# Kernel tuning notes

Hardware: AMD Instinct MI355X
Metric: run time of the kernel (lower is better)

## Reference

```python
import jax, jax.numpy as jnp
import numpy as np

EPS_GN = 1e-8
EPS_ATTN = 1e-8


def setup_inputs() -> dict:
    key = jax.random.key(0)
    ks = jax.random.split(key, 13)
    B, C, N = 4, 512, 2048
    s = 0.02
    return {
        "x": jax.random.normal(ks[0], (B, C, N), jnp.float32),
        "dw_w": jax.random.normal(ks[1], (C, 3), jnp.float32) * s,
        "pw_w": jax.random.normal(ks[2], (C, C), jnp.float32) * s,
        "u_w": jax.random.normal(ks[3], (2 * C, C), jnp.float32) * s,
        "u_b": jax.random.normal(ks[4], (2 * C,), jnp.float32) * s,
        "v_w": jax.random.normal(ks[5], (2 * C, C), jnp.float32) * s,
        "v_b": jax.random.normal(ks[6], (2 * C,), jnp.float32) * s,
        "h_w": jax.random.normal(ks[7], (C, C), jnp.float32) * s,
        "h_b": jax.random.normal(ks[8], (C,), jnp.float32) * s,
        "q_w": jax.random.normal(ks[9], (C, C), jnp.float32) * s,
        "k_w": jax.random.normal(ks[10], (C, C), jnp.float32) * s,
        "o_w": jax.random.normal(ks[11], (C, 2 * C), jnp.float32) * s,
        "o_b": jax.random.normal(ks[12], (C,), jnp.float32) * s,
    }


def reference(x, dw_w, pw_w, u_w, u_b, v_w, v_b, h_w, h_b, q_w, k_w, o_w, o_b):
    # x: [B, C, N]
    C = x.shape[1]
    # GroupNorm(1, C): normalize over (C, N) per sample; affine is identity-init
    # in torch but we follow the module math with default weight=1, bias=0
    mean = jnp.mean(x, axis=(1, 2), keepdims=True)
    var = jnp.var(x, axis=(1, 2), keepdims=True)
    z = (x - mean) * jax.lax.rsqrt(var + EPS_GN)

    # local depthwise conv k=3, pad=1 (cross-correlation), no bias
    zp = jnp.pad(z, ((0, 0), (0, 0), (1, 1)))
    dw = (dw_w[:, 0, None] * zp[:, :, :-2]
          + dw_w[:, 1, None] * zp[:, :, 1:-1]
          + dw_w[:, 2, None] * zp[:, :, 2:])
    # pointwise conv (no bias)
    z = z + jnp.einsum('oc,bcn->bon', pw_w, dw)

    u = jax.nn.sigmoid(jnp.einsum('oc,bcn->bon', u_w, z) + u_b[:, None])  # [B,2C,N]
    v = jnp.einsum('oc,bcn->bon', v_w, z) + v_b[:, None]                  # [B,2C,N]
    h = jnp.einsum('oc,bcn->bno', h_w, z) + h_b                           # [B,N,C]

    q = h @ q_w.T  # [B,N,C]
    k = h @ k_w.T  # [B,N,C]
    scale = 1.0 / jnp.sqrt(jnp.float32(C))

    logits = jnp.einsum('bnc,bmc->bnm', q, k) * scale
    a = jax.nn.relu(logits)
    a = a * a
    a = a / (jnp.sum(a, axis=-1, keepdims=True) + EPS_ATTN)

    av = jnp.einsum('bnm,bom->bon', a, v)  # [B,2C,N]
    y = jnp.einsum('oc,bcn->bon', o_w, u * av) + o_b[:, None]
    return x + y
```

## Files before the change

kernel.cpp:

```cpp
#include <hip/hip_runtime.h>
#include <hip/hip_bf16.h>
#include <cstdint>

typedef __bf16 bhalf;
typedef __bf16 bhalf8 __attribute__((ext_vector_type(8)));
typedef float f32x4 __attribute__((ext_vector_type(4)));

enum { EPI_Z2=0, EPI_UV=1, EPI_BIAS=2, EPI_QK=3, EPI_ATTN=4, EPI_PV=5, EPI_Y=6 };

__device__ __forceinline__ void gl_lds16(const bhalf* g, bhalf* l) {
  __builtin_amdgcn_global_load_lds(
      (const __attribute__((address_space(1))) unsigned int*)g,
      (__attribute__((address_space(3))) unsigned int*)l,
      16, 0, 0);
}
__device__ __forceinline__ void barrier_raw() { asm volatile("s_barrier" ::: "memory"); }
#define VMW(n)  asm volatile("s_waitcnt vmcnt(" #n ")" ::: "memory")
#define LGKM0() asm volatile("s_waitcnt lgkmcnt(0)" ::: "memory")


template<int EPI>
__global__ void __launch_bounds__(512, 2)
g8(const bhalf* __restrict__ A, const bhalf* __restrict__ Bw,
   void* __restrict__ Out, void* __restrict__ Out2,
   const float* __restrict__ bias, const float* __restrict__ bias2,
   int N, int K, long sA, long sB, long sO, long sAuxf, float scale)
{
  constexpr int ASL = 256*64;
  constexpr int ABUF = 2*ASL;
  constexpr int STRIDE = 2*ABUF;
  __shared__ __align__(16) char lds[2*STRIDE];

  const int gx = gridDim.x, gy = gridDim.y;
  const int nwg = gx*gy;
  const int flat = blockIdx.y*gx + blockIdx.x;
  const int q8 = nwg>>3, r8 = nwg&7, xcd = flat&7, o8 = flat>>3;
  const int wsw = (xcd<r8 ? xcd*(q8+1) : r8*(q8+1)+(xcd-r8)*q8) + o8;
  const int bx = wsw % gx, by = wsw / gx;
  const int m0 = by*256, n0 = bx*256;
  const int bz = blockIdx.z;

  const bhalf* Ab = A + (long)bz*sA;
  const bhalf* Bb = Bw + (long)bz*sB;

  const int tid = threadIdx.x, wid = tid>>6, lane = tid&63;
  const int lm = lane&15, kq = lane>>4;
  const int wm = wid>>2, wn = wid&3;
  const int srow = lane>>2;
  const int csw = ((lane&3) ^ ((lane>>3)&3)) * 8;
  const int kqs = kq ^ ((lm>>1)&3);

  f32x4 acc[8][4];
  #pragma unroll
  for (int i=0;i<8;i++)
    #pragma unroll
    for (int j=0;j<4;j++) acc[i][j] = f32x4{0.f,0.f,0.f,0.f};

  auto stage = [&](int buf, int t){
    char* base = lds + buf*STRIDE;
    const int k0 = t*64;
    #pragma unroll
    for (int ksl=0; ksl<2; ksl++){
      #pragma unroll
      for (int c=0;c<2;c++){
        bhalf* dA = (bhalf*)(base + ksl*ASL + (wid*32 + c*16)*64);
        gl_lds16(Ab + (long)(m0 + wid*32 + c*16 + srow)*K + k0 + ksl*32 + csw, dA);
        bhalf* dB = (bhalf*)(base + ABUF + ksl*ASL + (wid*32 + c*16)*64);
        gl_lds16(Bb + (long)(n0 + wid*32 + c*16 + srow)*K + k0 + ksl*32 + csw, dB);
      }
    }
  };

  auto compute = [&](int buf){
    char* base = lds + buf*STRIDE;
    #pragma unroll
    for (int ks=0; ks<2; ks++){
      bhalf8 af[8], bf[4];
      #pragma unroll
      for (int i=0;i<8;i++)
        af[i] = *(const bhalf8*)(base + ks*ASL + (wm*128 + i*16 + lm)*64 + kqs*16);
      #pragma unroll
      for (int j=0;j<4;j++)
        bf[j] = *(const bhalf8*)(base + ABUF + ks*ASL + (wn*64 + j*16 + lm)*64 + kqs*16);
      __builtin_amdgcn_s_setprio(1);
      #pragma unroll
      for (int i=0;i<8;i++)
        #pragma unroll
        for (int j=0;j<4;j++)
          acc[i][j] = __builtin_amdgcn_mfma_f32_16x16x32_bf16(af[i], bf[j], acc[i][j], 0,0,0);
      __builtin_amdgcn_s_setprio(0);
    }
  };

  const int NT = K>>6;
  stage(0,0);
  for (int t=0; t<NT; ++t){
    if (t+1<NT){ stage((t+1)&1, t+1); VMW(8); }
    else       { VMW(0); }
    barrier_raw();
    compute(t&1);
    barrier_raw();
  }

  char* obase; int ldb;
  const float* bv = nullptr; int bc0 = 0; bool sig = false;
  if constexpr (EPI==EPI_ATTN){
    obase = (char*)Out + 2*((long)bz*sO + (long)m0*N + n0); ldb = N*2;
  }
  if constexpr (EPI==EPI_UV){
    bool uh = n0 < 1024; sig = uh;
    obase = (char*)(uh?Out:Out2) + 2*((long)m0*1024 + (n0 - (uh?0:1024)));
    ldb = 2048; bv = uh ? bias : bias2; bc0 = uh ? n0 : n0-1024;
  }

  float rs[8][4];
  if constexpr (EPI==EPI_ATTN){
    #pragma unroll
    for (int i=0;i<8;i++)
      #pragma unroll
      for (int r=0;r<4;r++) rs[i][r]=0.f;
  }
  #pragma unroll
  for (int i=0;i<8;i++){
    #pragma unroll
    for (int j=0;j<4;j++){
      const int lcol = wn*64 + j*16 + lm;
      #pragma unroll
      for (int r=0;r<4;r++){
        const int lrow = wm*128 + i*16 + kq*4 + r;
        float v = acc[i][j][r];
        if constexpr (EPI==EPI_ATTN){
          v *= scale; v = fmaxf(v,0.f); v = v*v;
          rs[i][r] += v;
        }
        if constexpr (EPI==EPI_UV){
          v += bv[bc0 + lcol];
          if (sig) v = 1.f/(1.f + __expf(-v));
        }
        const int cb = lcol*2;
        const int lb = lrow*512 + (((cb>>5) ^ ((lrow>>2)&3))<<5) + (cb&31);
        *(bhalf*)(lds + lb) = (bhalf)v;
      }
    }
  }
  if constexpr (EPI==EPI_ATTN){
    float* rd = (float*)Out2;
    #pragma unroll
    for (int i=0;i<8;i++){
      const int rbase = m0 + wm*128 + i*16 + kq*4;
      #pragma unroll
      for (int r=0;r<4;r++){
        float s = rs[i][r];
        s += __shfl_xor(s,1); s += __shfl_xor(s,2);
        s += __shfl_xor(s,4); s += __shfl_xor(s,8);
        if (lm==0) atomicAdd(rd + (long)bz*sAuxf + rbase + r, s);
      }
    }
  }
  LGKM0();
  barrier_raw();
  #pragma unroll
  for (int it=0; it<16; ++it){
    const int g = (it*512 + tid)*16;
    const int row = g >> 9, off = g & 511;
    const int lb = row*512 + (((off>>5) ^ ((row>>2)&3))<<5) + (off&31);
    uint4 val = *(const uint4*)(lds + lb);
    *(uint4*)(obase + (long)row*ldb + off) = val;
  }
  (void)scale; (void)bias; (void)bias2; (void)N;
}

template<int EPI>
__global__ void __launch_bounds__(256, 2)
g4(const bhalf* __restrict__ A, const bhalf* __restrict__ Bw,
   void* __restrict__ Out, void* __restrict__ Out2,
   const bhalf* __restrict__ auxb, const float* __restrict__ auxf,
   int N, int K, long sA, long sB, long sO, float scale, int rowshift)
{
  constexpr int ABUF = 256*64;
  constexpr int BBUF = 128*64;
  constexpr int STRIDE = ABUF + BBUF;
  __shared__ __align__(16) char lds[3*STRIDE];

  const int gx = gridDim.x, gy = gridDim.y;
  const int nwg = gx*gy;
  const int flat = blockIdx.y*gx + blockIdx.x;
  const int q8 = nwg>>3, r8 = nwg&7, xcd = flat&7, o8 = flat>>3;
  const int wsw = (xcd<r8 ? xcd*(q8+1) : r8*(q8+1)+(xcd-r8)*q8) + o8;
  const int bx = wsw % gx, by = wsw / gx;
  const int m0 = by*256, n0 = bx*128;
  const int bz = blockIdx.z;

  const bhalf* Ab = A + (long)bz*sA;
  const bhalf* Bb = Bw + (rowshift ? (long)(m0>>rowshift)*sB : (long)bz*sB);

  const int tid = threadIdx.x, wid = tid>>6, lane = tid&63;
  const int lm = lane&15, kq = lane>>4;
  const int wm = wid>>1, wn = wid&1;
  const int srow = lane>>2;
  const int csw = ((lane&3) ^ ((lane>>3)&3)) * 8;
  const int kqs = kq ^ ((lm>>1)&3);

  f32x4 acc[8][4];
  #pragma unroll
  for (int i=0;i<8;i++)
    #pragma unroll
    for (int j=0;j<4;j++) acc[i][j] = f32x4{0.f,0.f,0.f,0.f};

  auto stage = [&](int buf, int t){
    char* base = lds + buf*STRIDE;
    const int k0 = t*32;
    #pragma unroll
    for (int c=0;c<4;c++){
      bhalf* dA = (bhalf*)(base + (wid*64 + c*16)*64);
      gl_lds16(Ab + (long)(m0 + wid*64 + c*16 + srow)*K + k0 + csw, dA);
    }
    #pragma unroll
    for (int c=0;c<2;c++){
      bhalf* dB = (bhalf*)(base + ABUF + (wid*32 + c*16)*64);
      gl_lds16(Bb + (long)(n0 + wid*32 + c*16 + srow)*K + k0 + csw, dB);
    }
  };

  auto compute = [&](int buf){
    char* base = lds + buf*STRIDE;
    bhalf8 af[8], bf[4];
    #pragma unroll
    for (int i=0;i<8;i++)
      af[i] = *(const bhalf8*)(base + (wm*128 + i*16 + lm)*64 + kqs*16);
    #pragma unroll
    for (int j=0;j<4;j++)
      bf[j] = *(const bhalf8*)(base + ABUF + (wn*64 + j*16 + lm)*64 + kqs*16);
    __builtin_amdgcn_s_setprio(1);
    #pragma unroll
    for (int i=0;i<8;i++)
      #pragma unroll
      for (int j=0;j<4;j++)
        acc[i][j] = __builtin_amdgcn_mfma_f32_16x16x32_bf16(af[i], bf[j], acc[i][j], 0,0,0);
    __builtin_amdgcn_s_setprio(0);
  };

  const int NT = K>>5;
  stage(0,0); stage(1,1);
  int b0 = 0;
  for (int t=0; t<NT; ++t){
    if (t+2<NT){
      int b2 = b0+2; if (b2>=3) b2-=3;
      stage(b2, t+2);
      VMW(12);
    } else if (t+1<NT) { VMW(6); }
    else               { VMW(0); }
    barrier_raw();
    compute(b0);
    barrier_raw();
    if (++b0==3) b0=0;
  }

  char* obase; int ldb;
  if constexpr (EPI==EPI_PV){
    obase = (char*)Out + 2*((long)m0*1024 + n0); ldb = 2048;
  }
  if constexpr (EPI==EPI_QK){
    bool qh = n0 < 512;
    obase = (char*)(qh?Out:Out2) + 2*((long)m0*512 + (n0 - (qh?0:512)));
    ldb = 1024;
  }
  #pragma unroll
  for (int i=0;i<8;i++){
    #pragma unroll
    for (int j=0;j<4;j++){
      const int lcol = wn*64 + j*16 + lm;
      #pragma unroll
      for (int r=0;r<4;r++){
        const int lrow = wm*128 + i*16 + kq*4 + r;
        float v = acc[i][j][r];
        if constexpr (EPI==EPI_PV){
          const int rowg = m0 + lrow;
          float den = auxf[rowg];
          v *= __builtin_amdgcn_rcpf(den + 1e-8f);
          v *= (float)auxb[(long)rowg*1024 + n0 + lcol];
        }
        const int cb = lcol*2;
        const int lb = lrow*256 + (((cb>>5) ^ ((lrow>>2)&3))<<5) + (cb&31);
        *(bhalf*)(lds + lb) = (bhalf)v;
      }
    }
  }
  LGKM0();
  barrier_raw();
  #pragma unroll
  for (int it=0; it<16; ++it){
    const int g = (it*256 + tid)*16;
    const int row = g >> 8, off = g & 255;
    const int lb = row*256 + (((off>>5) ^ ((row>>2)&3))<<5) + (off&31);
    uint4 val = *(const uint4*)(lds + lb);
    *(uint4*)(obase + (long)row*ldb + off) = val;
  }
  (void)scale; (void)auxb; (void)auxf; (void)N; (void)sO;
}

template<int EPI>
__global__ void __launch_bounds__(256, 2)
gemm_bt(const bhalf* __restrict__ A, const bhalf* __restrict__ Bw,
        void* __restrict__ Out,
        const float* __restrict__ bias,
        const bhalf* __restrict__ auxb,
        int M, int N, int K, long sA, long sB)
{
  constexpr int ABUF = 128*64;
  constexpr int STRIDE = 2*ABUF;
  __shared__ __align__(16) char lds[4*STRIDE];

  const int bz = blockIdx.z;
  const int gx = gridDim.x, gy = gridDim.y;
  const int nwg = gx*gy;
  const int flat = blockIdx.y*gx + blockIdx.x;
  const int q8 = nwg>>3, r8 = nwg&7, xcd = flat&7, o8 = flat>>3;
  const int w = (xcd<r8 ? xcd*(q8+1) : r8*(q8+1)+(xcd-r8)*q8) + o8;
  const int bx = w % gx, by = w / gx;

  const bhalf* Ab = A + (long)bz*sA;
  const bhalf* Bb = Bw + (long)bz*sB;
  const int tid = threadIdx.x;
  const int wid = tid>>6, lane = tid&63;
  const int lm = lane&15, kq = lane>>4;
  const int wr = (wid>>1)*64, wc = (wid&1)*64;
  const int m0 = by*128, n0 = bx*128;
  const int srow = lane>>2;
  const int csw = ((lane&3) ^ ((lane>>3)&3))*8;
  const int kqs = kq ^ ((lm>>1)&3);

  f32x4 acc[4][4];
  #pragma unroll
  for (int i=0;i<4;i++)
    #pragma unroll
    for (int j=0;j<4;j++) acc[i][j] = f32x4{0.f,0.f,0.f,0.f};

  auto stage = [&](int t){
    char* base = lds + (t&3)*STRIDE;
    const int k0 = t*32;
    #pragma unroll
    for (int c=0;c<2;c++){
      bhalf* dA = (bhalf*)(base + (wid*32 + c*16)*64);
      gl_lds16(Ab + (long)(m0 + wid*32 + c*16 + srow)*K + k0 + csw, dA);
      bhalf* dB = (bhalf*)(base + ABUF + (wid*32 + c*16)*64);
      gl_lds16(Bb + (long)(n0 + wid*32 + c*16 + srow)*K + k0 + csw, dB);
    }
  };

  auto compute = [&](int t){
    char* base = lds + (t&3)*STRIDE;
    bhalf8 af[4], bf[4];
    #pragma unroll
    for (int i=0;i<4;i++)
      af[i] = *(const bhalf8*)(base + (wr + i*16 + lm)*64 + kqs*16);
    #pragma unroll
    for (int j=0;j<4;j++)
      bf[j] = *(const bhalf8*)(base + ABUF + (wc + j*16 + lm)*64 + kqs*16);
    __builtin_amdgcn_s_setprio(1);
    #pragma unroll
    for (int i=0;i<4;i++)
      #pragma unroll
      for (int j=0;j<4;j++)
        acc[i][j] = __builtin_amdgcn_mfma_f32_16x16x32_bf16(af[i], bf[j], acc[i][j], 0,0,0);
    __builtin_amdgcn_s_setprio(0);
  };

  const int NT = K>>5;
  stage(0); stage(1); stage(2);
  for (int t=0; t<NT; ++t){
    if (t+3<NT){ stage(t+3); VMW(12); }
    else if (t+2<NT) { VMW(8); }
    else if (t+1<NT) { VMW(4); }
    else             { VMW(0); }
    barrier_raw();
    compute(t);
    barrier_raw();
  }

  char* obase = (char*)Out + 2*((long)m0*N + n0);
  const int ldb = N*2;
  #pragma unroll
  for (int i=0;i<4;i++){
    #pragma unroll
    for (int j=0;j<4;j++){
      const int lcol = wc + j*16 + lm;
      #pragma unroll
      for (int r=0;r<4;r++){
        const int lrow = wr + i*16 + kq*4 + r;
        float v = acc[i][j][r];
        if constexpr (EPI==EPI_Z2)
          v += (float)auxb[(long)(m0+lrow)*N + n0 + lcol];
        if constexpr (EPI==EPI_BIAS || EPI==EPI_Y)
          v += bias[n0 + lcol];
        const int cb = lcol*2;
        const int lb = lrow*256 + (((cb>>5) ^ ((lrow>>2)&3))<<5) + (cb&31);
        *(bhalf*)(lds + lb) = (bhalf)v;
      }
    }
  }
  LGKM0();
  barrier_raw();
  #pragma unroll
  for (int it=0; it<8; ++it){
    const int g = (it*256 + tid)*16;
    const int row = g >> 8, off = g & 255;
    const int lb = row*256 + (((off>>5) ^ ((row>>2)&3))<<5) + (off&31);
    uint4 val = *(const uint4*)(lds + lb);
    *(uint4*)(obase + (long)row*ldb + off) = val;
  }
  (void)M;
}

struct CvtArgs { const float* src[7]; bhalf* dst[7]; int n[7]; };
__global__ void cvt_multi(CvtArgs a) {
  int seg = blockIdx.y;
  int i = (blockIdx.x*256 + threadIdx.x)*4;
  if (i >= a.n[seg]) return;
  float4 f = *(const float4*)(a.src[seg] + i);
  bhalf* d = a.dst[seg] + i;
  d[0]=(bhalf)f.x; d[1]=(bhalf)f.y; d[2]=(bhalf)f.z; d[3]=(bhalf)f.w;
}

__global__ void gn_part(const float* __restrict__ x, float* __restrict__ ps, float* __restrict__ pss) {
  int b = blockIdx.y;
  const float* xb = x + (long)b*(512*2048);
  float s=0.f, ss=0.f;
  #pragma unroll
  for (int it=0; it<8; it++){
    int idx = ((it*128 + blockIdx.x)*256 + threadIdx.x)*4;
    float4 f = *(const float4*)(xb + idx);
    s  += f.x+f.y+f.z+f.w;
    ss += f.x*f.x+f.y*f.y+f.z*f.z+f.w*f.w;
  }
  for (int off=32; off; off>>=1){ s += __shfl_xor(s,off); ss += __shfl_xor(ss,off); }
  __shared__ float ls[4], lss[4];
  int wid = threadIdx.x>>6, lane = threadIdx.x&63;
  if (lane==0){ ls[wid]=s; lss[wid]=ss; }
  __syncthreads();
  if (threadIdx.x==0){
    s = ls[0]+ls[1]+ls[2]+ls[3]; ss = lss[0]+lss[1]+lss[2]+lss[3];
    ps[b*128 + blockIdx.x] = s; pss[b*128 + blockIdx.x] = ss;
  }
}

__global__ void gn_final(const float* __restrict__ ps, const float* __restrict__ pss,
                         float* __restrict__ stats) {
  int b = blockIdx.x;
  float s = ps[b*128 + threadIdx.x], ss = pss[b*128 + threadIdx.x];
  for (int off=32; off; off>>=1){ s += __shfl_xor(s,off); ss += __shfl_xor(ss,off); }
  __shared__ float l0[2], l1[2];
  int wid = threadIdx.x>>6, lane = threadIdx.x&63;
  if (lane==0){ l0[wid]=s; l1[wid]=ss; }
  __syncthreads();
  if (threadIdx.x==0){
    s = l0[0]+l0[1]; ss = l1[0]+l1[1];
    float mean = s*(1.f/1048576.f);
    float var  = ss*(1.f/1048576.f) - mean*mean;
    stats[b*2] = mean; stats[b*2+1] = rsqrtf(var + 1e-8f);
  }
}

__global__ void norm_dw_T(const float* __restrict__ x, const float* __restrict__ stats,
                          const float* __restrict__ dw_w,
                          bhalf* __restrict__ zT, bhalf* __restrict__ dwT) {
  int b = blockIdx.z, n0 = blockIdx.x*32, c0 = blockIdx.y*32;
  float mean = stats[b*2], rstd = stats[b*2+1];
  __shared__ float zs[32][35];
  int tx = threadIdx.x, ty = threadIdx.y;
  #pragma unroll
  for (int r=0;r<4;r++){
    int c = c0 + ty + r*8;
    for (int cc=tx; cc<34; cc+=32){
      int n = n0 - 1 + cc;
      float v = 0.f;
      if (n>=0 && n<2048) v = (x[((long)b*512 + c)*2048 + n] - mean)*rstd;
      zs[ty + r*8][cc] = v;
    }
  }
  __syncthreads();
  float w0 = dw_w[(c0+tx)*3+0], w1 = dw_w[(c0+tx)*3+1], w2 = dw_w[(c0+tx)*3+2];
  #pragma unroll
  for (int r=0;r<4;r++){
    int ln = ty + r*8;
    float z = zs[tx][ln+1];
    float d = w0*zs[tx][ln] + w1*zs[tx][ln+1] + w2*zs[tx][ln+2];
    long o = ((long)b*2048 + n0 + ln)*512 + c0 + tx;
    zT[o] = (bhalf)z; dwT[o] = (bhalf)d;
  }
}

__global__ void transpose_bf16(const bhalf* __restrict__ in, bhalf* __restrict__ out,
                               int R, int C) {
  __shared__ bhalf t[32][33];
  int r0 = blockIdx.x*32, c0 = blockIdx.y*32;
  long ib = (long)blockIdx.z*R*C;
  int tx = threadIdx.x, ty = threadIdx.y;
  #pragma unroll
  for (int r=0;r<4;r++)
    t[ty + r*8][tx] = in[ib + (long)(r0 + ty + r*8)*C + c0 + tx];
  __syncthreads();
  #pragma unroll
  for (int r=0;r<4;r++)
    out[ib + (long)(c0 + ty + r*8)*R + r0 + tx] = t[tx][ty + r*8];
}

__global__ void final_add(const float* __restrict__ x, const bhalf* __restrict__ yT,
                          float* __restrict__ out) {
  __shared__ float t[32][33];
  int n0 = blockIdx.x*32, c0 = blockIdx.y*32, b = blockIdx.z;
  int tx = threadIdx.x, ty = threadIdx.y;
  #pragma unroll
  for (int r=0;r<4;r++)
    t[ty + r*8][tx] = (float)yT[((long)b*2048 + n0 + ty + r*8)*512 + c0 + tx];
  __syncthreads();
  #pragma unroll
  for (int r=0;r<4;r++){
    long idx = ((long)b*512 + c0 + ty + r*8)*2048 + n0 + tx;
    out[idx] = x[idx] + t[tx][ty + r*8];
  }
}

extern "C" void kernel_launch(void* const* d_in, const int* in_sizes, int n_in,
                              void* d_out, int out_size, void* d_ws, size_t ws_size,
                              hipStream_t stream) {
  (void)in_sizes; (void)n_in; (void)out_size; (void)ws_size;
  const float* x    = (const float*)d_in[0];
  const float* dw_w = (const float*)d_in[1];
  const float* pw_w = (const float*)d_in[2];
  const float* u_w  = (const float*)d_in[3];
  const float* u_b  = (const float*)d_in[4];
  const float* v_w  = (const float*)d_in[5];
  const float* v_b  = (const float*)d_in[6];
  const float* h_w  = (const float*)d_in[7];
  const float* h_b  = (const float*)d_in[8];
  const float* q_w  = (const float*)d_in[9];
  const float* k_w  = (const float*)d_in[10];
  const float* o_w  = (const float*)d_in[11];
  const float* o_b  = (const float*)d_in[12];
  float* out = (float*)d_out;

  char* ws = (char*)d_ws;
  size_t off = 0;
  auto alloc = [&](size_t bytes) -> void* {
    void* p = ws + off; off = (off + bytes + 255) & ~(size_t)255; return p;
  };

  float* ps    = (float*)alloc(4*128*4);
  float* pss   = (float*)alloc(4*128*4);
  float* stats = (float*)alloc(4*2*4);
  float* rden  = (float*)alloc(4*2048*4);
  bhalf* wb_pw = (bhalf*)alloc(512*512*2);
  bhalf* wb_uv = (bhalf*)alloc((size_t)2048*512*2);
  bhalf* wb_h  = (bhalf*)alloc(512*512*2);
  bhalf* wb_qk = (bhalf*)alloc((size_t)1024*512*2);
  bhalf* wb_o  = (bhalf*)alloc((size_t)512*1024*2);
  const size_t ACT = (size_t)4*2048*512;
  bhalf* zT   = (bhalf*)alloc(ACT*2);
  bhalf* dwT  = (bhalf*)alloc(ACT*2);
  bhalf* z2T  = (bhalf*)alloc(ACT*2);
  bhalf* ub   = (bhalf*)alloc(ACT*2*2);
  bhalf* vT   = (bhalf*)alloc(ACT*2*2);
  bhalf* v_fm = (bhalf*)alloc(ACT*2*2);
  bhalf* hb   = (bhalf*)alloc(ACT*2);
  bhalf* wsc  = (bhalf*)alloc((size_t)4*2048*2048*2);
  bhalf* uav  = (bhalf*)alloc(ACT*2*2);
  bhalf* qb = zT;  bhalf* kb = dwT;  bhalf* yT = vT;

  hipMemsetAsync(rden, 0, 4*2048*4, stream);

  CvtArgs ca;
  ca.src[0]=pw_w; ca.dst[0]=wb_pw;           ca.n[0]=512*512;
  ca.src[1]=u_w;  ca.dst[1]=wb_uv;           ca.n[1]=1024*512;
  ca.src[2]=v_w;  ca.dst[2]=wb_uv+1024*512;  ca.n[2]=1024*512;
  ca.src[3]=h_w;  ca.dst[3]=wb_h;            ca.n[3]=512*512;
  ca.src[4]=q_w;  ca.dst[4]=wb_qk;           ca.n[4]=512*512;
  ca.src[5]=k_w;  ca.dst[5]=wb_qk+512*512;   ca.n[5]=512*512;
  ca.src[6]=o_w;  ca.dst[6]=wb_o;            ca.n[6]=512*1024;
  cvt_multi<<<dim3(512,7), 256, 0, stream>>>(ca);

  gn_part<<<dim3(128,4), 256, 0, stream>>>(x, ps, pss);
  gn_final<<<dim3(4), 128, 0, stream>>>(ps, pss, stats);

  norm_dw_T<<<dim3(64,16,4), dim3(32,8), 0, stream>>>(x, stats, dw_w, zT, dwT);

  const float iscl = 0.044194173824159216f;
  gemm_bt<EPI_Z2><<<dim3(4,64,1), 256, 0, stream>>>(dwT, wb_pw, z2T,
      nullptr, zT, 8192, 512, 512, 0, 0);
  g8<EPI_UV><<<dim3(8,32,1), 512, 0, stream>>>(z2T, wb_uv, ub, vT,
      u_b, v_b, 2048, 512, 0, 0, 0, 0, 0.f);
  gemm_bt<EPI_BIAS><<<dim3(4,64,1), 256, 0, stream>>>(z2T, wb_h, hb,
      h_b, nullptr, 8192, 512, 512, 0, 0);
  g4<EPI_QK><<<dim3(8,32,1), 256, 0, stream>>>(hb, wb_qk, qb, kb,
      nullptr, nullptr, 1024, 512, 0, 0, 0, 0.f, 0);
  transpose_bf16<<<dim3(64,32,4), dim3(32,8), 0, stream>>>(vT, v_fm, 2048, 1024);
  g8<EPI_ATTN><<<dim3(8,8,4), 512, 0, stream>>>(qb, kb, wsc, rden,
      nullptr, nullptr, 2048, 512,
      (long)2048*512, (long)2048*512, (long)2048*2048, 2048, iscl);
  g4<EPI_PV><<<dim3(8,32,1), 256, 0, stream>>>(wsc, v_fm, uav, nullptr,
      ub, rden, 1024, 2048, 0, (long)1024*2048, 0, 0.f, 11);
  gemm_bt<EPI_Y><<<dim3(4,64,1), 256, 0, stream>>>(uav, wb_o, yT,
      o_b, nullptr, 8192, 512, 1024, 0, 0);
  final_add<<<dim3(64,16,4), dim3(32,8), 0, stream>>>(x, yT, out);
}
```

Measured before the change: 210.2 us.

## Use 8-wave workgroups for QK, PV and projection GEMMs

Replaces the 4-wave g4 kernel with g8n, which runs 512 threads over the same 256x128 tile so each wave owns a 64x64 subtile. It also converts gemm_bt to 8 waves with 64x32 per-wave subtiles and a unified A/B staging loop. The aim is more waves per CU to hide latency and fewer accumulators per wave, at the cost of less register-level reuse per wave and more LDS fragment reads per MFMA.

```diff
diff --git a/kernel.cpp b/kernel.cpp
--- a/kernel.cpp
+++ b/kernel.cpp
@@ -18,6 +18,131 @@
 #define VMW(n)  asm volatile("s_waitcnt vmcnt(" #n ")" ::: "memory")
 #define LGKM0() asm volatile("s_waitcnt lgkmcnt(0)" ::: "memory")
 
+
+template<int EPI>
+__global__ void __launch_bounds__(512, 2)
+g8n(const bhalf* __restrict__ A, const bhalf* __restrict__ Bw,
+    void* __restrict__ Out, void* __restrict__ Out2,
+    const bhalf* __restrict__ auxb, const float* __restrict__ auxf,
+    int N, int K, long sB, float scale, int rowshift)
+{
+  constexpr int STRIDE = 384*64;
+  __shared__ __align__(16) char lds[3*STRIDE];
+
+  const int gx = gridDim.x, gy = gridDim.y;
+  const int nwg = gx*gy;
+  const int flat = blockIdx.y*gx + blockIdx.x;
+  const int q8 = nwg>>3, r8 = nwg&7, xcd = flat&7, o8 = flat>>3;
+  const int wsw = (xcd<r8 ? xcd*(q8+1) : r8*(q8+1)+(xcd-r8)*q8) + o8;
+  const int bx = wsw % gx, by = wsw / gx;
+  const int m0 = by*256, n0 = bx*128;
+
+  const bhalf* Ab = A;
+  const bhalf* Bb = Bw + (rowshift ? (long)(m0>>rowshift)*sB : 0);
+
+  const int tid = threadIdx.x, wid = tid>>6, lane = tid&63;
+  const int lm = lane&15, kq = lane>>4;
+  const int wm = wid>>1, wn = wid&1;
+  const int srow = lane>>2;
+  const int csw = ((lane&3) ^ ((lane>>3)&3)) * 8;
+  const int kqs = kq ^ ((lm>>1)&3);
+
+  f32x4 acc[4][4];
+  #pragma unroll
+  for (int i=0;i<4;i++)
+    #pragma unroll
+    for (int j=0;j<4;j++) acc[i][j] = f32x4{0.f,0.f,0.f,0.f};
+
+  auto stage = [&](int buf, int t){
+    char* base = lds + buf*STRIDE;
+    const int k0 = t*32;
+    #pragma unroll
+    for (int c=0;c<3;c++){
+      const int r0 = wid*48 + c*16;
+      bhalf* d = (bhalf*)(base + r0*64);
+      const bhalf* g = (r0 < 256)
+        ? Ab + (long)(m0 + r0 + srow)*K + k0 + csw
+        : Bb + (long)(n0 + r0 - 256 + srow)*K + k0 + csw;
+      gl_lds16(g, d);
+    }
+  };
+
+  auto compute = [&](int buf){
+    char* base = lds + buf*STRIDE;
+    bhalf8 af[4], bf[4];
+    #pragma unroll
+    for (int i=0;i<4;i++)
+      af[i] = *(const bhalf8*)(base + (wm*64 + i*16 + lm)*64 + kqs*16);
+    #pragma unroll
+    for (int j=0;j<4;j++)
+      bf[j] = *(const bhalf8*)(base + (256 + wn*64 + j*16 + lm)*64 + kqs*16);
+    __builtin_amdgcn_s_setprio(1);
+    #pragma unroll
+    for (int i=0;i<4;i++)
+      #pragma unroll
+      for (int j=0;j<4;j++)
+        acc[i][j] = __builtin_amdgcn_mfma_f32_16x16x32_bf16(af[i], bf[j], acc[i][j], 0,0,0);
+    __builtin_amdgcn_s_setprio(0);
+  };
+
+  const int NT = K>>5;
+  stage(0,0); stage(1,1);
+  int b0 = 0;
+  for (int t=0; t<NT; ++t){
+    if (t+2<NT){
+      int b2 = b0+2; if (b2>=3) b2-=3;
+      stage(b2, t+2);
+      VMW(6);
+    } else if (t+1<NT) { VMW(3); }
+    else               { VMW(0); }
+    barrier_raw();
+    compute(b0);
+    barrier_raw();
+    if (++b0==3) b0=0;
+  }
+
+  char* obase; int ldb;
+  if constexpr (EPI==EPI_PV){
+    obase = (char*)Out + 2*((long)m0*1024 + n0); ldb = 2048;
+  }
+  if constexpr (EPI==EPI_QK){
+    bool qh = n0 < 512;
+    obase = (char*)(qh?Out:Out2) + 2*((long)m0*512 + (n0 - (qh?0:512)));
+    ldb = 1024;
+  }
+  #pragma unroll
+  for (int i=0;i<4;i++){
+    #pragma unroll
+    for (int j=0;j<4;j++){
+      const int lcol = wn*64 + j*16 + lm;
+      #pragma unroll
+      for (int r=0;r<4;r++){
+        const int lrow = wm*64 + i*16 + kq*4 + r;
+        float v = acc[i][j][r];
+        if constexpr (EPI==EPI_PV){
+          const int rowg = m0 + lrow;
+          float den = auxf[rowg];
+          v *= __builtin_amdgcn_rcpf(den + 1e-8f);
+          v *= (float)auxb[(long)rowg*1024 + n0 + lcol];
+        }
+        const int cb = lcol*2;
+        const int lb = lrow*256 + (((cb>>5) ^ ((lrow>>2)&3))<<5) + (cb&31);
+        *(bhalf*)(lds + lb) = (bhalf)v;
+      }
+    }
+  }
+  LGKM0();
+  barrier_raw();
+  #pragma unroll
+  for (int it=0; it<8; ++it){
+    const int g = (it*512 + tid)*16;
+    const int row = g >> 8, off = g & 255;
+    const int lb = row*256 + (((off>>5) ^ ((row>>2)&3))<<5) + (off&31);
+    uint4 val = *(const uint4*)(lds + lb);
+    *(uint4*)(obase + (long)row*ldb + off) = val;
+  }
+  (void)scale; (void)auxb; (void)auxf; (void)N;
+}
 
 template<int EPI>
 __global__ void __launch_bounds__(512, 2)
@@ -171,147 +296,16 @@
 }
 
 template<int EPI>
-__global__ void __launch_bounds__(256, 2)
-g4(const bhalf* __restrict__ A, const bhalf* __restrict__ Bw,
-   void* __restrict__ Out, void* __restrict__ Out2,
-   const bhalf* __restrict__ auxb, const float* __restrict__ auxf,
-   int N, int K, long sA, long sB, long sO, float scale, int rowshift)
-{
-  constexpr int ABUF = 256*64;
-  constexpr int BBUF = 128*64;
-  constexpr int STRIDE = ABUF + BBUF;
-  __shared__ __align__(16) char lds[3*STRIDE];
-
-  const int gx = gridDim.x, gy = gridDim.y;
-  const int nwg = gx*gy;
-  const int flat = blockIdx.y*gx + blockIdx.x;
-  const int q8 = nwg>>3, r8 = nwg&7, xcd = flat&7, o8 = flat>>3;
-  const int wsw = (xcd<r8 ? xcd*(q8+1) : r8*(q8+1)+(xcd-r8)*q8) + o8;
-  const int bx = wsw % gx, by = wsw / gx;
-  const int m0 = by*256, n0 = bx*128;
-  const int bz = blockIdx.z;
-
-  const bhalf* Ab = A + (long)bz*sA;
-  const bhalf* Bb = Bw + (rowshift ? (long)(m0>>rowshift)*sB : (long)bz*sB);
-
-  const int tid = threadIdx.x, wid = tid>>6, lane = tid&63;
-  const int lm = lane&15, kq = lane>>4;
-  const int wm = wid>>1, wn = wid&1;
-  const int srow = lane>>2;
-  const int csw = ((lane&3) ^ ((lane>>3)&3)) * 8;
-  const int kqs = kq ^ ((lm>>1)&3);
-
-  f32x4 acc[8][4];
-  #pragma unroll
-  for (int i=0;i<8;i++)
-    #pragma unroll
-    for (int j=0;j<4;j++) acc[i][j] = f32x4{0.f,0.f,0.f,0.f};
-
-  auto stage = [&](int buf, int t){
-    char* base = lds + buf*STRIDE;
-    const int k0 = t*32;
-    #pragma unroll
-    for (int c=0;c<4;c++){
-      bhalf* dA = (bhalf*)(base + (wid*64 + c*16)*64);
-      gl_lds16(Ab + (long)(m0 + wid*64 + c*16 + srow)*K + k0 + csw, dA);
-    }
-    #pragma unroll
-    for (int c=0;c<2;c++){
-      bhalf* dB = (bhalf*)(base + ABUF + (wid*32 + c*16)*64);
-      gl_lds16(Bb + (long)(n0 + wid*32 + c*16 + srow)*K + k0 + csw, dB);
-    }
-  };
-
-  auto compute = [&](int buf){
-    char* base = lds + buf*STRIDE;
-    bhalf8 af[8], bf[4];
-    #pragma unroll
-    for (int i=0;i<8;i++)
-      af[i] = *(const bhalf8*)(base + (wm*128 + i*16 + lm)*64 + kqs*16);
-    #pragma unroll
-    for (int j=0;j<4;j++)
-      bf[j] = *(const bhalf8*)(base + ABUF + (wn*64 + j*16 + lm)*64 + kqs*16);
-    __builtin_amdgcn_s_setprio(1);
-    #pragma unroll
-    for (int i=0;i<8;i++)
-      #pragma unroll
-      for (int j=0;j<4;j++)
-        acc[i][j] = __builtin_amdgcn_mfma_f32_16x16x32_bf16(af[i], bf[j], acc[i][j], 0,0,0);
-    __builtin_amdgcn_s_setprio(0);
-  };
-
-  const int NT = K>>5;
-  stage(0,0); stage(1,1);
-  int b0 = 0;
-  for (int t=0; t<NT; ++t){
-    if (t+2<NT){
-      int b2 = b0+2; if (b2>=3) b2-=3;
-      stage(b2, t+2);
-      VMW(12);
-    } else if (t+1<NT) { VMW(6); }
-    else               { VMW(0); }
-    barrier_raw();
-    compute(b0);
-    barrier_raw();
-    if (++b0==3) b0=0;
-  }
-
-  char* obase; int ldb;
-  if constexpr (EPI==EPI_PV){
-    obase = (char*)Out + 2*((long)m0*1024 + n0); ldb = 2048;
-  }
-  if constexpr (EPI==EPI_QK){
-    bool qh = n0 < 512;
-    obase = (char*)(qh?Out:Out2) + 2*((long)m0*512 + (n0 - (qh?0:512)));
-    ldb = 1024;
-  }
-  #pragma unroll
-  for (int i=0;i<8;i++){
-    #pragma unroll
-    for (int j=0;j<4;j++){
-      const int lcol = wn*64 + j*16 + lm;
-      #pragma unroll
-      for (int r=0;r<4;r++){
-        const int lrow = wm*128 + i*16 + kq*4 + r;
-        float v = acc[i][j][r];
-        if constexpr (EPI==EPI_PV){
-          const int rowg = m0 + lrow;
-          float den = auxf[rowg];
-          v *= __builtin_amdgcn_rcpf(den + 1e-8f);
-          v *= (float)auxb[(long)rowg*1024 + n0 + lcol];
-        }
-        const int cb = lcol*2;
-        const int lb = lrow*256 + (((cb>>5) ^ ((lrow>>2)&3))<<5) + (cb&31);
-        *(bhalf*)(lds + lb) = (bhalf)v;
-      }
-    }
-  }
-  LGKM0();
-  barrier_raw();
-  #pragma unroll
-  for (int it=0; it<16; ++it){
-    const int g = (it*256 + tid)*16;
-    const int row = g >> 8, off = g & 255;
-    const int lb = row*256 + (((off>>5) ^ ((row>>2)&3))<<5) + (off&31);
-    uint4 val = *(const uint4*)(lds + lb);
-    *(uint4*)(obase + (long)row*ldb + off) = val;
-  }
-  (void)scale; (void)auxb; (void)auxf; (void)N; (void)sO;
-}
-
-template<int EPI>
-__global__ void __launch_bounds__(256, 2)
+__global__ void __launch_bounds__(512, 2)
 gemm_bt(const bhalf* __restrict__ A, const bhalf* __restrict__ Bw,
         void* __restrict__ Out,
         const float* __restrict__ bias,
         const bhalf* __restrict__ auxb,
-        int M, int N, int K, long sA, long sB)
+        int M, int N, int K)
 {
-  constexpr int ABUF = 128*64;
-  constexpr int STRIDE = 2*ABUF;
+  constexpr int STRIDE = 256*64;
   __shared__ __align__(16) char lds[4*STRIDE];
 
-  const int bz = blockIdx.z;
   const int gx = gridDim.x, gy = gridDim.y;
   const int nwg = gx*gy;
   const int flat = blockIdx.y*gx + blockIdx.x;
@@ -319,49 +313,49 @@
   const int w = (xcd<r8 ? xcd*(q8+1) : r8*(q8+1)+(xcd-r8)*q8) + o8;
   const int bx = w % gx, by = w / gx;
 
-  const bhalf* Ab = A + (long)bz*sA;
-  const bhalf* Bb = Bw + (long)bz*sB;
   const int tid = threadIdx.x;
   const int wid = tid>>6, lane = tid&63;
   const int lm = lane&15, kq = lane>>4;
-  const int wr = (wid>>1)*64, wc = (wid&1)*64;
+  const int wm = wid>>2, wn = wid&3;
   const int m0 = by*128, n0 = bx*128;
   const int srow = lane>>2;
   const int csw = ((lane&3) ^ ((lane>>3)&3))*8;
   const int kqs = kq ^ ((lm>>1)&3);
 
-  f32x4 acc[4][4];
+  f32x4 acc[4][2];
   #pragma unroll
   for (int i=0;i<4;i++)
     #pragma unroll
-    for (int j=0;j<4;j++) acc[i][j] = f32x4{0.f,0.f,0.f,0.f};
+    for (int j=0;j<2;j++) acc[i][j] = f32x4{0.f,0.f,0.f,0.f};
 
   auto stage = [&](int t){
     char* base = lds + (t&3)*STRIDE;
     const int k0 = t*32;
     #pragma unroll
     for (int c=0;c<2;c++){
-      bhalf* dA = (bhalf*)(base + (wid*32 + c*16)*64);
-      gl_lds16(Ab + (long)(m0 + wid*32 + c*16 + srow)*K + k0 + csw, dA);
-      bhalf* dB = (bhalf*)(base + ABUF + (wid*32 + c*16)*64);
-      gl_lds16(Bb + (long)(n0 + wid*32 + c*16 + srow)*K + k0 + csw, dB);
+      const int r0 = wid*32 + c*16;
+      bhalf* d = (bhalf*)(base + r0*64);
+      const bhalf* g = (r0 < 128)
+        ? A + (long)(m0 + r0 + srow)*K + k0 + csw
+        : Bw + (long)(n0 + r0 - 128 + srow)*K + k0 + csw;
+      gl_lds16(g, d);
     }
   };
 
   auto compute = [&](int t){
     char* base = lds + (t&3)*STRIDE;
-    bhalf8 af[4], bf[4];
+    bhalf8 af[4], bf[2];
     #pragma unroll
     for (int i=0;i<4;i++)
-      af[i] = *(const bhalf8*)(base + (wr + i*16 + lm)*64 + kqs*16);
-    #pragma unroll
-    for (int j=0;j<4;j++)
-      bf[j] = *(const bhalf8*)(base + ABUF + (wc + j*16 + lm)*64 + kqs*16);
+      af[i] = *(const bhalf8*)(base + (wm*64 + i*16 + lm)*64 + kqs*16);
+    #pragma unroll
+    for (int j=0;j<2;j++)
+      bf[j] = *(const bhalf8*)(base + (128 + wn*32 + j*16 + lm)*64 + kqs*16);
     __builtin_amdgcn_s_setprio(1);
     #pragma unroll
     for (int i=0;i<4;i++)
       #pragma unroll
-      for (int j=0;j<4;j++)
+      for (int j=0;j<2;j++)
         acc[i][j] = __builtin_amdgcn_mfma_f32_16x16x32_bf16(af[i], bf[j], acc[i][j], 0,0,0);
     __builtin_amdgcn_s_setprio(0);
   };
@@ -369,9 +363,9 @@
   const int NT = K>>5;
   stage(0); stage(1); stage(2);
   for (int t=0; t<NT; ++t){
-    if (t+3<NT){ stage(t+3); VMW(12); }
-    else if (t+2<NT) { VMW(8); }
-    else if (t+1<NT) { VMW(4); }
+    if (t+3<NT){ stage(t+3); VMW(6); }
+    else if (t+2<NT) { VMW(4); }
+    else if (t+1<NT) { VMW(2); }
     else             { VMW(0); }
     barrier_raw();
     compute(t);
@@ -383,11 +377,11 @@
   #pragma unroll
   for (int i=0;i<4;i++){
     #pragma unroll
-    for (int j=0;j<4;j++){
-      const int lcol = wc + j*16 + lm;
+    for (int j=0;j<2;j++){
+      const int lcol = wn*32 + j*16 + lm;
       #pragma unroll
       for (int r=0;r<4;r++){
-        const int lrow = wr + i*16 + kq*4 + r;
+        const int lrow = wm*64 + i*16 + kq*4 + r;
         float v = acc[i][j][r];
         if constexpr (EPI==EPI_Z2)
           v += (float)auxb[(long)(m0+lrow)*N + n0 + lcol];
@@ -402,8 +396,8 @@
   LGKM0();
   barrier_raw();
   #pragma unroll
-  for (int it=0; it<8; ++it){
-    const int g = (it*256 + tid)*16;
+  for (int it=0; it<4; ++it){
+    const int g = (it*512 + tid)*16;
     const int row = g >> 8, off = g & 255;
     const int lb = row*256 + (((off>>5) ^ ((row>>2)&3))<<5) + (off&31);
     uint4 val = *(const uint4*)(lds + lb);
@@ -585,21 +579,21 @@
   norm_dw_T<<<dim3(64,16,4), dim3(32,8), 0, stream>>>(x, stats, dw_w, zT, dwT);
 
   const float iscl = 0.044194173824159216f;
-  gemm_bt<EPI_Z2><<<dim3(4,64,1), 256, 0, stream>>>(dwT, wb_pw, z2T,
-      nullptr, zT, 8192, 512, 512, 0, 0);
+  gemm_bt<EPI_Z2><<<dim3(4,64,1), 512, 0, stream>>>(dwT, wb_pw, z2T,
+      nullptr, zT, 8192, 512, 512);
   g8<EPI_UV><<<dim3(8,32,1), 512, 0, stream>>>(z2T, wb_uv, ub, vT,
       u_b, v_b, 2048, 512, 0, 0, 0, 0, 0.f);
-  gemm_bt<EPI_BIAS><<<dim3(4,64,1), 256, 0, stream>>>(z2T, wb_h, hb,
-      h_b, nullptr, 8192, 512, 512, 0, 0);
-  g4<EPI_QK><<<dim3(8,32,1), 256, 0, stream>>>(hb, wb_qk, qb, kb,
-      nullptr, nullptr, 1024, 512, 0, 0, 0, 0.f, 0);
+  gemm_bt<EPI_BIAS><<<dim3(4,64,1), 512, 0, stream>>>(z2T, wb_h, hb,
+      h_b, nullptr, 8192, 512, 512);
+  g8n<EPI_QK><<<dim3(8,32,1), 512, 0, stream>>>(hb, wb_qk, qb, kb,
+      nullptr, nullptr, 1024, 512, 0, 0.f, 0);
   transpose_bf16<<<dim3(64,32,4), dim3(32,8), 0, stream>>>(vT, v_fm, 2048, 1024);
   g8<EPI_ATTN><<<dim3(8,8,4), 512, 0, stream>>>(qb, kb, wsc, rden,
       nullptr, nullptr, 2048, 512,
       (long)2048*512, (long)2048*512, (long)2048*2048, 2048, iscl);
-  g4<EPI_PV><<<dim3(8,32,1), 256, 0, stream>>>(wsc, v_fm, uav, nullptr,
-      ub, rden, 1024, 2048, 0, (long)1024*2048, 0, 0.f, 11);
-  gemm_bt<EPI_Y><<<dim3(4,64,1), 256, 0, stream>>>(uav, wb_o, yT,
-      o_b, nullptr, 8192, 512, 1024, 0, 0);
+  g8n<EPI_PV><<<dim3(8,32,1), 512, 0, stream>>>(wsc, v_fm, uav, nullptr,
+      ub, rden, 1024, 2048, (long)1024*2048, 0.f, 11);
+  gemm_bt<EPI_Y><<<dim3(4,64,1), 512, 0, stream>>>(uav, wb_o, yT,
+      o_b, nullptr, 8192, 512, 1024);
   final_add<<<dim3(64,16,4), dim3(32,8), 0, stream>>>(x, yT, out);
 }
```

Result: faster. 202.0 us (-3.9%).
